# Kernel optimization log

Hardware: AMD Instinct MI355X
Metric: run time of the kernel (lower is better)

The kernel has to match this reference:

```python
import jax, jax.numpy as jnp
import numpy as np

F_FACETS = 400000
TEX_PER = 4            # textures per facet (counts sum must equal total textures)
T_TEX = F_FACETS * TEX_PER
C_IN = 64
C_OUT = 64
L = 2
N_BASIS = (L + 1) ** 2  # 9
BN_EPS = 1e-3


def setup_inputs() -> dict:
    key = jax.random.key(0)
    k1, k2, k3 = jax.random.split(key, 3)
    input_texture = jax.random.normal(k1, (T_TEX, C_IN), jnp.float32)
    bary_coeff = jax.random.uniform(k2, (T_TEX, N_BASIS), jnp.float32)
    # per-facet texture counts; constant 4 so counts sum exactly to T_TEX
    num_texture = jnp.full((F_FACETS,), TEX_PER, dtype=jnp.int32)
    # xavier_normal_ on [O, I, K]: fan_in = I*K, fan_out = ... torch uses fan_in=I*K? For 3D it treats dim1*rest.
    std = float(np.sqrt(2.0 / (C_IN * N_BASIS + C_OUT * N_BASIS)))
    weights = jax.random.normal(k3, (C_OUT, C_IN, N_BASIS), jnp.float32) * std
    biases = jnp.zeros((1, C_OUT), jnp.float32)
    gamma = jnp.ones((C_OUT,), jnp.float32)
    beta = jnp.zeros((C_OUT,), jnp.float32)
    return {
        "input_texture": input_texture,
        "bary_coeff": bary_coeff,
        "weights": weights,
        "biases": biases,
        "gamma": gamma,
        "beta": beta,
        "num_texture": num_texture,
    }


def reference(input_texture, bary_coeff, weights, biases, gamma, beta, num_texture):
    T = input_texture.shape[0]
    n_facets = num_texture.shape[0]
    n_basis = weights.shape[2]
    # per-texture contribution: contrib[t,o] = sum_{i,k} x[t,i] * W[o,i,k] * bary[t,k]
    # loop over small fixed basis count (9) to avoid a [T, I, K] intermediate
    contrib = jnp.zeros((T, weights.shape[0]), dtype=input_texture.dtype)
    for k in range(n_basis):
        contrib = contrib + (input_texture @ weights[:, :, k].T) * bary_coeff[:, k:k + 1]
    # scatter-sum per facet (ragged groups given by num_texture), then average
    seg_ids = jnp.repeat(jnp.arange(n_facets), num_texture, total_repeat_length=T)
    facet_sum = jax.ops.segment_sum(contrib, seg_ids, num_segments=n_facets)
    out = facet_sum / num_texture[:, None].astype(facet_sum.dtype)
    # bias + ReLU
    out = jax.nn.relu(out + biases)
    # BatchNorm1d in training mode: batch stats (biased variance), eps=1e-3
    mu = jnp.mean(out, axis=0)
    var = jnp.mean(jnp.square(out - mu), axis=0)
    out = (out - mu) * jax.lax.rsqrt(var + BN_EPS) * gamma + beta
    return out
```

## Files before the change

### kernel.cpp

```cpp
#include <hip/hip_runtime.h>


typedef _Float16 half8  __attribute__((ext_vector_type(8)));
typedef _Float16 h2     __attribute__((ext_vector_type(2)));
typedef __fp16   fp16x2 __attribute__((ext_vector_type(2)));
typedef float    f32x4  __attribute__((ext_vector_type(4)));
typedef float    f32x16 __attribute__((ext_vector_type(16)));

#define NQUADS  25000
#define FFACETS 400000
#define GRID1   512
#define LDSP    18752

#define WAITV(N) asm volatile("s_waitcnt vmcnt(" #N ")" ::: "memory")
#define WAITL0() asm volatile("s_waitcnt lgkmcnt(0)" ::: "memory")
#define FENCE()  asm volatile("" ::: "memory")

union H8 { h2 h[4]; half8 v; };

static __device__ __forceinline__ h2 pkrtz(float a, float b) {
    fp16x2 r = __builtin_amdgcn_cvt_pkrtz(a, b);
    return __builtin_bit_cast(h2, r);
}

static __device__ __forceinline__ float qsum(float s) {
    s += __builtin_bit_cast(float, __builtin_amdgcn_mov_dpp(
             __builtin_bit_cast(int, s), 0xB1, 0xF, 0xF, true));
    s += __builtin_bit_cast(float, __builtin_amdgcn_mov_dpp(
             __builtin_bit_cast(int, s), 0x4E, 0xF, 0xF, true));
    return s;
}

static __device__ __forceinline__ void gload16(const void* g, void* l) {
    __builtin_amdgcn_global_load_lds((const __attribute__((address_space(1))) void*)g,
                                     (__attribute__((address_space(3))) void*)l, 16, 0, 0);
}

__global__ __launch_bounds__(256) void prep_kernel(const float* __restrict__ W,
                                                   _Float16* __restrict__ wswz,
                                                   float* __restrict__ stats) {
    int idx = blockIdx.x * 256 + threadIdx.x;
    if (idx < 36864) {
        int j    = idx & 7;
        int lane = (idx >> 3) & 63;
        int wc   = (idx >> 9) & 1;
        int c    = idx >> 10;
        int o    = wc * 32 + (lane & 31);
        int i    = (c & 3) * 16 + (lane >> 5) * 8 + j;
        int kb   = c >> 2;
        wswz[idx] = (_Float16)W[(o * 64 + i) * 9 + kb];
    }
    if (idx < 128) stats[idx] = 0.0f;
}

__global__ __launch_bounds__(256, 2) void pass1_kernel(
    const float* __restrict__ X, const float* __restrict__ BARY,
    const _Float16* __restrict__ WSWZ, const float* __restrict__ BIAS,
    const int* __restrict__ NTEX, float* __restrict__ OUT,
    float* __restrict__ stats) {

    __shared__ __align__(16) char ldsbuf[3 * LDSP];
    __shared__ float sl_s[128];
    __shared__ float sl_s2[128];
    __shared__ float sbias[64];

    const int tid  = threadIdx.x;
    const int wave = tid >> 6;
    const int lane = tid & 63;
    const int wc   = wave >> 1;
    const int wt   = wave & 1;
    const int t    = lane & 31;
    const int hi   = lane >> 5;
    const int q    = lane & 3;

    sbias[lane] = BIAS[lane];
    WAITL0();

    half8 wf[36];
#pragma unroll
    for (int c = 0; c < 36; ++c)
        wf[c] = *(const half8*)(WSWZ + ((size_t)(c * 2 + wc) * 64 + lane) * 8);

    int xsg[4];
#pragma unroll
    for (int i = 0; i < 4; ++i) {
        const int tt = wave * 16 + i * 4 + (lane >> 4);
        xsg[i] = tt * 256 + (((lane & 15) ^ (tt & 15)) << 4);
    }
    const int xd = wave * 4096 + lane * 16;
    const char* Xb  = (const char*)X;
    const char* BAb = (const char*)BARY;
    const char* NTb = (const char*)NTEX;

    int xr[8];
#pragma unroll
    for (int ciq = 0; ciq < 4; ++ciq)
#pragma unroll
        for (int jj = 0; jj < 2; ++jj)
            xr[ciq * 2 + jj] = (wt * 32 + t) * 256 +
                               (((ciq * 4 + hi * 2 + jj) ^ (lane & 15)) << 4);
    const int bco = 16384 + (wt * 2 + (t >> 4)) * 576 + (lane & 15) * 36;
    const int nco = 18688 + wt * 32 + ((t >> 2) << 2);

    float sacc[4]  = {0.f, 0.f, 0.f, 0.f};
    float s2acc[4] = {0.f, 0.f, 0.f, 0.f};

    const int b = blockIdx.x;
    const int n = (NQUADS - 1 - b) / GRID1 + 1;

    auto STAGE = [&](char* S, int u) {
        const char* xs = Xb + (size_t)u * 16384;
        FENCE();
        gload16(xs + xsg[0], S + xd);
        gload16(xs + xsg[1], S + xd + 1024);
        gload16(xs + xsg[2], S + xd + 2048);
        gload16(xs + xsg[3], S + xd + 3072);
        if (lane < 36) gload16(BAb + (size_t)u * 2304 + wave * 576 + lane * 16,
                               S + 16384 + wave * 576 + lane * 16);
        if (lane < 1)  gload16(NTb + (size_t)u * 64 + wave * 16, S + 18688 + wave * 16);
        FENCE();
    };

    auto ITER = [&](const char* L, char* S, int u, int upre, bool do_stage) {
        __builtin_amdgcn_s_barrier();
        FENCE();
        f32x4 r[8];
#pragma unroll
        for (int k = 0; k < 8; ++k) r[k] = *(const f32x4*)(L + xr[k]);
        float bF[9];
#pragma unroll
        for (int k = 0; k < 9; ++k) bF[k] = *(const float*)(L + bco + k * 4);
        const int nt = *(const int*)(L + nco);
        f32x4 bias4[4];
#pragma unroll
        for (int qp = 0; qp < 4; ++qp)
            bias4[qp] = *(const f32x4*)&sbias[wc * 32 + hi * 4 + qp * 8];

        if (do_stage) STAGE(S, upre);

        h2 xh[16], bh[9];
#pragma unroll
        for (int k = 0; k < 8; ++k) {
            xh[k * 2]     = pkrtz(r[k][0], r[k][1]);
            xh[k * 2 + 1] = pkrtz(r[k][2], r[k][3]);
        }
#pragma unroll
        for (int k = 0; k < 9; ++k) bh[k] = pkrtz(bF[k], bF[k]);
        const float rc = __builtin_amdgcn_rcpf((float)nt);

        f32x16 acc = {};
        __builtin_amdgcn_s_setprio(1);
#pragma unroll
        for (int c = 0; c < 36; ++c) {
            const h2 bk = bh[c >> 2];
            const int xb = (c & 3) * 4;
            H8 bf;
            bf.h[0] = xh[xb + 0] * bk;  bf.h[1] = xh[xb + 1] * bk;
            bf.h[2] = xh[xb + 2] * bk;  bf.h[3] = xh[xb + 3] * bk;
            acc = __builtin_amdgcn_mfma_f32_32x32x16_f16(wf[c], bf.v, acc, 0, 0, 0);
        }
        __builtin_amdgcn_s_setprio(0);

        f32x4 vq[4];
#pragma unroll
        for (int qp = 0; qp < 4; ++qp)
#pragma unroll
            for (int j = 0; j < 4; ++j) {
                float s = qsum(acc[qp * 4 + j]);
                s = s * rc + bias4[qp][j];
                vq[qp][j] = s > 0.f ? s : 0.f;
            }

#pragma unroll
        for (int j = 0; j < 4; ++j) {
            float p = vq[0][j];
            p = (q == 1) ? vq[1][j] : p;
            p = (q == 2) ? vq[2][j] : p;
            p = (q == 3) ? vq[3][j] : p;
            sacc[j]  += p;
            s2acc[j] += p * p;
        }

        const int f = u * 16 + wt * 8 + (t >> 2);
        if ((lane & 3) == 0) {
            float* op = OUT + (size_t)f * 64 + wc * 32 + hi * 4;
            *(f32x4*)(op)      = vq[0];
            *(f32x4*)(op + 8)  = vq[1];
            *(f32x4*)(op + 16) = vq[2];
            *(f32x4*)(op + 24) = vq[3];
        }
    };

    char* B0 = ldsbuf;
    char* B1 = ldsbuf + LDSP;
    char* B2 = ldsbuf + 2 * LDSP;

    STAGE(B0, b);
    STAGE(B1, b + GRID1);
    WAITV(6);  ITER(B0, B2, b,         b + 2 * GRID1, true);
    WAITV(10); ITER(B1, B0, b + GRID1, b + 3 * GRID1, true);
    char *rd = B2, *st = B1, *ot = B0;
    int tI = 2;
    for (; tI < n - 2; ++tI) {
        WAITV(14);
        ITER(rd, st, b + tI * GRID1, b + (tI + 2) * GRID1, true);
        char* tmp = ot; ot = st; st = rd; rd = tmp;
    }
    WAITV(14); ITER(rd, st, b + tI * GRID1, 0, false);
    { char* tmp = ot; ot = st; st = rd; rd = tmp; } ++tI;
    WAITV(8);  ITER(rd, st, b + tI * GRID1, 0, false);

#pragma unroll
    for (int j = 0; j < 4; ++j) {
        float s = sacc[j], s2 = s2acc[j];
        s  += __shfl_xor(s, 4);   s  += __shfl_xor(s, 8);   s  += __shfl_xor(s, 16);
        s2 += __shfl_xor(s2, 4);  s2 += __shfl_xor(s2, 8);  s2 += __shfl_xor(s2, 16);
        if (((lane >> 2) & 7) == 0) {
            const int idx = wt * 64 + wc * 32 + hi * 4 + q * 8 + j;
            sl_s[idx]  = s;
            sl_s2[idx] = s2;
        }
    }
    __syncthreads();
    if (tid < 64)        atomicAdd(&stats[tid], sl_s[tid] + sl_s[tid + 64]);
    else if (tid < 128)  atomicAdd(&stats[tid], sl_s2[tid - 64] + sl_s2[tid]);
}

__global__ __launch_bounds__(256) void pass3_kernel(float* __restrict__ OUT,
    const float* __restrict__ stats, const float* __restrict__ gamma,
    const float* __restrict__ beta) {
    const int tid = threadIdx.x;
    const size_t l = (size_t)blockIdx.x * 256 + tid;
    const int c0 = ((int)l & 15) * 4;
    float mu[4], sc[4], be[4];
    const float invF = 1.0f / (float)FFACETS;
#pragma unroll
    for (int u = 0; u < 4; ++u) {
        int ch = c0 + u;
        float m  = stats[ch] * invF;
        float va = stats[64 + ch] * invF - m * m;
        mu[u] = m;
        sc[u] = rsqrtf(va + 1e-3f) * gamma[ch];
        be[u] = beta[ch];
    }
    const size_t n4 = (size_t)FFACETS * 16;
    for (size_t i = l; i < n4; i += (size_t)gridDim.x * 256) {
        f32x4 v = ((f32x4*)OUT)[i];
#pragma unroll
        for (int u = 0; u < 4; ++u)
            v[u] = (v[u] - mu[u]) * sc[u] + be[u];
        ((f32x4*)OUT)[i] = v;
    }
}

extern "C" void kernel_launch(void* const* d_in, const int* in_sizes, int n_in,
                              void* d_out, int out_size, void* d_ws, size_t ws_size,
                              hipStream_t stream) {
    const float* X     = (const float*)d_in[0];
    const float* BARY  = (const float*)d_in[1];
    const float* W     = (const float*)d_in[2];
    const float* BIAS  = (const float*)d_in[3];
    const float* GAMMA = (const float*)d_in[4];
    const float* BETA  = (const float*)d_in[5];
    const int*   NTEX  = (const int*)d_in[6];
    float* OUT = (float*)d_out;

    _Float16* wswz = (_Float16*)d_ws;
    float* stats   = (float*)((char*)d_ws + 73728);

    prep_kernel<<<144, 256, 0, stream>>>(W, wswz, stats);
    pass1_kernel<<<GRID1, 256, 0, stream>>>(X, BARY, wswz, BIAS, NTEX, OUT, stats);
    pass3_kernel<<<2048, 256, 0, stream>>>(OUT, stats, GAMMA, BETA);
}
```

Before: 653.3 us.

## Split K across wave pairs to halve weight registers and raise occupancy

Each block now processes 32 textures (8 facets) per step instead of 64. The 36 MFMA K-chunks are split between two waves, each holding 18 weight fragments instead of 36. Partial accumulators are swapped through an LDS exchange buffer with an extra barrier, and each wave finalizes half of the output channels. Smaller LDS staging and register footprint allow 3 blocks per CU and a grid of 768, raising occupancy to hide memory latency, at the cost of an extra LDS round-trip and barrier per iteration.

```diff
diff --git a/kernel.cpp b/kernel.cpp
--- a/kernel.cpp
+++ b/kernel.cpp
@@ -7,10 +7,10 @@
 typedef float    f32x4  __attribute__((ext_vector_type(4)));
 typedef float    f32x16 __attribute__((ext_vector_type(16)));
 
-#define NQUADS  25000
+#define NPAIRS  50000
 #define FFACETS 400000
-#define GRID1   512
-#define LDSP    18752
+#define GRID1   768
+#define LDSP    9472
 
 #define WAITV(N) asm volatile("s_waitcnt vmcnt(" #N ")" ::: "memory")
 #define WAITL0() asm volatile("s_waitcnt lgkmcnt(0)" ::: "memory")
@@ -53,96 +53,87 @@
     if (idx < 128) stats[idx] = 0.0f;
 }
 
-__global__ __launch_bounds__(256, 2) void pass1_kernel(
+__global__ __launch_bounds__(256, 3) void pass1_kernel(
     const float* __restrict__ X, const float* __restrict__ BARY,
     const _Float16* __restrict__ WSWZ, const float* __restrict__ BIAS,
     const int* __restrict__ NTEX, float* __restrict__ OUT,
     float* __restrict__ stats) {
 
     __shared__ __align__(16) char ldsbuf[3 * LDSP];
-    __shared__ float sl_s[128];
-    __shared__ float sl_s2[128];
-    __shared__ float sbias[64];
+    __shared__ __align__(16) char xchg[8192];
+    __shared__ float sl_s[64];
+    __shared__ float sl_s2[64];
 
     const int tid  = threadIdx.x;
     const int wave = tid >> 6;
     const int lane = tid & 63;
     const int wc   = wave >> 1;
-    const int wt   = wave & 1;
+    const int wk   = wave & 1;
     const int t    = lane & 31;
     const int hi   = lane >> 5;
-    const int q    = lane & 3;
-
-    sbias[lane] = BIAS[lane];
-    WAITL0();
-
-    half8 wf[36];
-#pragma unroll
-    for (int c = 0; c < 36; ++c)
-        wf[c] = *(const half8*)(WSWZ + ((size_t)(c * 2 + wc) * 64 + lane) * 8);
-
-    int xsg[4];
-#pragma unroll
-    for (int i = 0; i < 4; ++i) {
-        const int tt = wave * 16 + i * 4 + (lane >> 4);
+
+    half8 wf[18];
+#pragma unroll
+    for (int cc = 0; cc < 18; ++cc)
+        wf[cc] = *(const half8*)(WSWZ + ((size_t)((2 * cc + wk) * 2 + wc) * 64 + lane) * 8);
+
+    const f32x4 bias0 = *(const f32x4*)(BIAS + wc * 32 + wk * 16 + 4 * hi);
+    const f32x4 bias1 = *(const f32x4*)(BIAS + wc * 32 + wk * 16 + 8 + 4 * hi);
+
+    int xsg[2], xdd[2];
+#pragma unroll
+    for (int i = 0; i < 2; ++i) {
+        const int tt = wave * 8 + i * 4 + (lane >> 4);
         xsg[i] = tt * 256 + (((lane & 15) ^ (tt & 15)) << 4);
-    }
-    const int xd = wave * 4096 + lane * 16;
+        xdd[i] = wave * 2048 + i * 1024 + lane * 16;
+    }
     const char* Xb  = (const char*)X;
     const char* BAb = (const char*)BARY;
     const char* NTb = (const char*)NTEX;
 
-    int xr[8];
-#pragma unroll
-    for (int ciq = 0; ciq < 4; ++ciq)
-#pragma unroll
-        for (int jj = 0; jj < 2; ++jj)
-            xr[ciq * 2 + jj] = (wt * 32 + t) * 256 +
-                               (((ciq * 4 + hi * 2 + jj) ^ (lane & 15)) << 4);
-    const int bco = 16384 + (wt * 2 + (t >> 4)) * 576 + (lane & 15) * 36;
-    const int nco = 18688 + wt * 32 + ((t >> 2) << 2);
-
-    float sacc[4]  = {0.f, 0.f, 0.f, 0.f};
-    float s2acc[4] = {0.f, 0.f, 0.f, 0.f};
+    int xr[4];
+#pragma unroll
+    for (int g = 0; g < 4; ++g) {
+        const int gg = (wk + 2 * (g >> 1)) * 4 + hi * 2 + (g & 1);
+        xr[g] = t * 256 + ((gg ^ (t & 15)) << 4);
+    }
+    const int bco = 8192 + t * 36;
+    const int nco = 9344 + ((t >> 2) << 2);
+
+    float sacc0 = 0.f, s2acc0 = 0.f, sacc1 = 0.f, s2acc1 = 0.f;
 
     const int b = blockIdx.x;
-    const int n = (NQUADS - 1 - b) / GRID1 + 1;
+    const int n = (NPAIRS - 1 - b) / GRID1 + 1;
 
     auto STAGE = [&](char* S, int u) {
-        const char* xs = Xb + (size_t)u * 16384;
-        FENCE();
-        gload16(xs + xsg[0], S + xd);
-        gload16(xs + xsg[1], S + xd + 1024);
-        gload16(xs + xsg[2], S + xd + 2048);
-        gload16(xs + xsg[3], S + xd + 3072);
-        if (lane < 36) gload16(BAb + (size_t)u * 2304 + wave * 576 + lane * 16,
-                               S + 16384 + wave * 576 + lane * 16);
-        if (lane < 1)  gload16(NTb + (size_t)u * 64 + wave * 16, S + 18688 + wave * 16);
+        const char* xs = Xb + (size_t)u * 8192;
+        FENCE();
+        gload16(xs + xsg[0], S + xdd[0]);
+        gload16(xs + xsg[1], S + xdd[1]);
+        gload16(BAb + (size_t)u * 1152 + lane * 16, S + 8192 + lane * 16);
+        if (lane < 8) gload16(BAb + (size_t)u * 1152 + 1024 + lane * 16, S + 9216 + lane * 16);
+        if (lane < 2) gload16(NTb + (size_t)u * 32 + lane * 16,          S + 9344 + lane * 16);
         FENCE();
     };
 
     auto ITER = [&](const char* L, char* S, int u, int upre, bool do_stage) {
         __builtin_amdgcn_s_barrier();
         FENCE();
-        f32x4 r[8];
-#pragma unroll
-        for (int k = 0; k < 8; ++k) r[k] = *(const f32x4*)(L + xr[k]);
+        f32x4 r[4];
+#pragma unroll
+        for (int g = 0; g < 4; ++g) r[g] = *(const f32x4*)(L + xr[g]);
         float bF[9];
 #pragma unroll
         for (int k = 0; k < 9; ++k) bF[k] = *(const float*)(L + bco + k * 4);
         const int nt = *(const int*)(L + nco);
-        f32x4 bias4[4];
-#pragma unroll
-        for (int qp = 0; qp < 4; ++qp)
-            bias4[qp] = *(const f32x4*)&sbias[wc * 32 + hi * 4 + qp * 8];
 
         if (do_stage) STAGE(S, upre);
 
-        h2 xh[16], bh[9];
-#pragma unroll
-        for (int k = 0; k < 8; ++k) {
-            xh[k * 2]     = pkrtz(r[k][0], r[k][1]);
-            xh[k * 2 + 1] = pkrtz(r[k][2], r[k][3]);
+        h2 xh[8], bh[9];
+#pragma unroll
+        for (int g = 0; g < 4; ++g) {
+            xh[g * 2]     = pkrtz(r[g][0], r[g][1]);
+            xh[g * 2 + 1] = pkrtz(r[g][2], r[g][3]);
         }
 #pragma unroll
         for (int k = 0; k < 9; ++k) bh[k] = pkrtz(bF[k], bF[k]);
@@ -151,43 +142,62 @@
         f32x16 acc = {};
         __builtin_amdgcn_s_setprio(1);
 #pragma unroll
-        for (int c = 0; c < 36; ++c) {
-            const h2 bk = bh[c >> 2];
-            const int xb = (c & 3) * 4;
+        for (int cc = 0; cc < 18; ++cc) {
+            const h2 bk = bh[cc >> 1];
+            const int bs = (cc & 1) * 4;
             H8 bf;
-            bf.h[0] = xh[xb + 0] * bk;  bf.h[1] = xh[xb + 1] * bk;
-            bf.h[2] = xh[xb + 2] * bk;  bf.h[3] = xh[xb + 3] * bk;
-            acc = __builtin_amdgcn_mfma_f32_32x32x16_f16(wf[c], bf.v, acc, 0, 0, 0);
+            bf.h[0] = xh[bs + 0] * bk;  bf.h[1] = xh[bs + 1] * bk;
+            bf.h[2] = xh[bs + 2] * bk;  bf.h[3] = xh[bs + 3] * bk;
+            acc = __builtin_amdgcn_mfma_f32_32x32x16_f16(wf[cc], bf.v, acc, 0, 0, 0);
         }
         __builtin_amdgcn_s_setprio(0);
 
-        f32x4 vq[4];
-#pragma unroll
-        for (int qp = 0; qp < 4; ++qp)
-#pragma unroll
-            for (int j = 0; j < 4; ++j) {
-                float s = qsum(acc[qp * 4 + j]);
-                s = s * rc + bias4[qp][j];
-                vq[qp][j] = s > 0.f ? s : 0.f;
-            }
-
+        f32x4 wlo, whi, mlo, mhi;
+        if (wk == 0) {
+            wlo = (f32x4){acc[8],  acc[9],  acc[10], acc[11]};
+            whi = (f32x4){acc[12], acc[13], acc[14], acc[15]};
+            mlo = (f32x4){acc[0],  acc[1],  acc[2],  acc[3]};
+            mhi = (f32x4){acc[4],  acc[5],  acc[6],  acc[7]};
+        } else {
+            wlo = (f32x4){acc[0],  acc[1],  acc[2],  acc[3]};
+            whi = (f32x4){acc[4],  acc[5],  acc[6],  acc[7]};
+            mlo = (f32x4){acc[8],  acc[9],  acc[10], acc[11]};
+            mhi = (f32x4){acc[12], acc[13], acc[14], acc[15]};
+        }
+        char* slotW = xchg + (size_t)(wc * 2 + wk) * 2048;
+        *(f32x4*)(slotW + lane * 16)        = wlo;
+        *(f32x4*)(slotW + 1024 + lane * 16) = whi;
+        WAITL0();
+        __builtin_amdgcn_s_barrier();
+        FENCE();
+        const char* slotR = xchg + (size_t)(wc * 2 + (1 - wk)) * 2048;
+        f32x4 plo = *(const f32x4*)(slotR + lane * 16);
+        f32x4 phi = *(const f32x4*)(slotR + 1024 + lane * 16);
+
+        const int f = u * 8 + (t >> 2);
+        f32x4 vq0, vq1;
 #pragma unroll
         for (int j = 0; j < 4; ++j) {
-            float p = vq[0][j];
-            p = (q == 1) ? vq[1][j] : p;
-            p = (q == 2) ? vq[2][j] : p;
-            p = (q == 3) ? vq[3][j] : p;
-            sacc[j]  += p;
-            s2acc[j] += p * p;
-        }
-
-        const int f = u * 16 + wt * 8 + (t >> 2);
+            float s0 = qsum(mlo[j] + plo[j]);
+            float s1 = qsum(mhi[j] + phi[j]);
+            s0 = s0 * rc + bias0[j];
+            s1 = s1 * rc + bias1[j];
+            vq0[j] = s0 > 0.f ? s0 : 0.f;
+            vq1[j] = s1 > 0.f ? s1 : 0.f;
+        }
+        {
+            const int q = lane & 3;
+            float p0 = vq0[0]; p0 = (q == 1) ? vq0[1] : p0;
+            p0 = (q == 2) ? vq0[2] : p0;  p0 = (q == 3) ? vq0[3] : p0;
+            float p1 = vq1[0]; p1 = (q == 1) ? vq1[1] : p1;
+            p1 = (q == 2) ? vq1[2] : p1;  p1 = (q == 3) ? vq1[3] : p1;
+            sacc0 += p0;  s2acc0 += p0 * p0;
+            sacc1 += p1;  s2acc1 += p1 * p1;
+        }
         if ((lane & 3) == 0) {
-            float* op = OUT + (size_t)f * 64 + wc * 32 + hi * 4;
-            *(f32x4*)(op)      = vq[0];
-            *(f32x4*)(op + 8)  = vq[1];
-            *(f32x4*)(op + 16) = vq[2];
-            *(f32x4*)(op + 24) = vq[3];
+            float* op = OUT + (size_t)f * 64 + wc * 32 + wk * 16 + 4 * hi;
+            *(f32x4*)(op)     = vq0;
+            *(f32x4*)(op + 8) = vq1;
         }
     };
 
@@ -197,33 +207,34 @@
 
     STAGE(B0, b);
     STAGE(B1, b + GRID1);
-    WAITV(6);  ITER(B0, B2, b,         b + 2 * GRID1, true);
-    WAITV(10); ITER(B1, B0, b + GRID1, b + 3 * GRID1, true);
+    WAITV(5); ITER(B0, B2, b,         b + 2 * GRID1, true);
+    WAITV(7); ITER(B1, B0, b + GRID1, b + 3 * GRID1, true);
     char *rd = B2, *st = B1, *ot = B0;
     int tI = 2;
     for (; tI < n - 2; ++tI) {
-        WAITV(14);
+        WAITV(9);
         ITER(rd, st, b + tI * GRID1, b + (tI + 2) * GRID1, true);
         char* tmp = ot; ot = st; st = rd; rd = tmp;
     }
-    WAITV(14); ITER(rd, st, b + tI * GRID1, 0, false);
+    WAITV(9); ITER(rd, st, b + tI * GRID1, 0, false);
     { char* tmp = ot; ot = st; st = rd; rd = tmp; } ++tI;
-    WAITV(8);  ITER(rd, st, b + tI * GRID1, 0, false);
-
-#pragma unroll
-    for (int j = 0; j < 4; ++j) {
-        float s = sacc[j], s2 = s2acc[j];
-        s  += __shfl_xor(s, 4);   s  += __shfl_xor(s, 8);   s  += __shfl_xor(s, 16);
-        s2 += __shfl_xor(s2, 4);  s2 += __shfl_xor(s2, 8);  s2 += __shfl_xor(s2, 16);
-        if (((lane >> 2) & 7) == 0) {
-            const int idx = wt * 64 + wc * 32 + hi * 4 + q * 8 + j;
-            sl_s[idx]  = s;
-            sl_s2[idx] = s2;
+    WAITV(4); ITER(rd, st, b + tI * GRID1, 0, false);
+
+    {
+        float s0 = sacc0, q0 = s2acc0, s1 = sacc1, q1 = s2acc1;
+        s0 += __shfl_xor(s0, 4);  s0 += __shfl_xor(s0, 8);  s0 += __shfl_xor(s0, 16);
+        q0 += __shfl_xor(q0, 4);  q0 += __shfl_xor(q0, 8);  q0 += __shfl_xor(q0, 16);
+        s1 += __shfl_xor(s1, 4);  s1 += __shfl_xor(s1, 8);  s1 += __shfl_xor(s1, 16);
+        q1 += __shfl_xor(q1, 4);  q1 += __shfl_xor(q1, 8);  q1 += __shfl_xor(q1, 16);
+        if ((lane & 28) == 0) {
+            const int ch0 = wc * 32 + wk * 16 + 4 * hi + (lane & 3);
+            sl_s [ch0]     = s0;  sl_s2[ch0]     = q0;
+            sl_s [ch0 + 8] = s1;  sl_s2[ch0 + 8] = q1;
         }
     }
     __syncthreads();
-    if (tid < 64)        atomicAdd(&stats[tid], sl_s[tid] + sl_s[tid + 64]);
-    else if (tid < 128)  atomicAdd(&stats[tid], sl_s2[tid - 64] + sl_s2[tid]);
+    if (tid < 64)        atomicAdd(&stats[tid],      sl_s [tid]);
+    else if (tid < 128)  atomicAdd(&stats[tid],      sl_s2[tid - 64]);
 }
 
 __global__ __launch_bounds__(256) void pass3_kernel(float* __restrict__ OUT,
```

Measured after the change: 657.4 us. No clear change (+0.6%).
